# Kernel optimization log

Measured on AMD Instinct MI355X. Metric: run time of the kernel, lower is better.

The kernel has to match this reference:

```python
import jax, jax.numpy as jnp
import numpy as np

B, L, E, H, NL = 2, 1024, 1024, 16, 3
D = E // H
SCALE = D ** -0.5
EPS = 1e-5


def rmsnorm(x, g):
    return x * jax.lax.rsqrt(jnp.mean(x * x, axis=-1, keepdims=True) + EPS) * g


def rope(x, cos, sin):
    # x: (B, m*L, H, D); cos/sin: (L, D). Tile cos/sin to the growing KV length
    # (the source broadcasts rel_pos over the concatenated cache).
    m = x.shape[1] // cos.shape[0]
    c = jnp.tile(cos, (m, 1))[None, :, None, :]
    s = jnp.tile(sin, (m, 1))[None, :, None, :]
    x1, x2 = jnp.split(x, 2, axis=-1)
    rot = jnp.concatenate([-x2, x1], axis=-1)  # rotate_half convention
    return x * c + rot * s


def setup_inputs() -> dict:
    key = jax.random.key(0)
    ks = jax.random.split(key, 8)
    x = jax.random.normal(ks[0], (B, L, E), jnp.float32)
    inv_freq = 1.0 / (10000.0 ** (jnp.arange(0, D, 2, dtype=jnp.float32) / D))
    t = jnp.arange(L, dtype=jnp.float32)[:, None] * inv_freq[None, :]  # (L, D/2)
    cos = jnp.concatenate([jnp.cos(t), jnp.cos(t)], axis=-1)
    sin = jnp.concatenate([jnp.sin(t), jnp.sin(t)], axis=-1)
    attn_mask = jnp.where(jnp.tril(jnp.ones((L, L), bool)), 0.0, -jnp.inf).astype(jnp.float32)
    w_scale = E ** -0.5  # ~kaiming_uniform fan_in magnitude
    Wq = jax.random.normal(ks[1], (NL, E, E), jnp.float32) * w_scale
    Wk = jax.random.normal(ks[2], (NL, E, E), jnp.float32) * w_scale
    Wv = jax.random.normal(ks[3], (NL, E, E), jnp.float32) * w_scale
    Wo = jax.random.normal(ks[4], (E, E), jnp.float32) * w_scale
    lambdas = jax.random.normal(ks[5], (NL,), jnp.float32)
    g_ln = jnp.ones((NL, E), jnp.float32)
    g_final = jnp.ones((E,), jnp.float32)
    alpha = jnp.ones((1,), jnp.float32)
    return dict(x=x, cos=cos, sin=sin, attn_mask=attn_mask, Wq=Wq, Wk=Wk, Wv=Wv,
                g_ln=g_ln, lambdas=lambdas, Wo=Wo, g_final=g_final, alpha=alpha)


def reference(x, cos, sin, attn_mask, Wq, Wk, Wv, g_ln, lambdas, Wo, g_final, alpha):
    # lambda weights: sigmoid then non-affine LayerNorm across the NL layers
    s = jax.nn.sigmoid(lambdas)
    lw = (s - s.mean()) * jax.lax.rsqrt(s.var() + EPS)

    acc_k, acc_v = [], []
    outs = []
    for i in range(NL):
        q = (x @ Wq[i].T).reshape(B, L, H, D)
        k = (x @ Wk[i].T).reshape(B, L, H, D)
        v = (x @ Wv[i].T).reshape(B, L, H, D)
        if i > 0:  # prepend-current growing KV cache (source concatenates [k, accumulated])
            k = jnp.concatenate([k] + acc_k, axis=1)
            v = jnp.concatenate([v] + acc_v, axis=1)
        q = rope(q, cos, sin)
        k = rope(k, cos, sin)
        KV = k.shape[1]
        scores = jnp.einsum('bqhd,bkhd->bhqk', q * SCALE, k)  # (B,H,L,KV)
        if i == 0:
            m = attn_mask
        else:  # source fills everything past tgt_len with -inf
            m = jnp.concatenate(
                [attn_mask, jnp.full((L, KV - L), -jnp.inf, attn_mask.dtype)], axis=1)
        w = jax.nn.softmax(scores + m, axis=-1)
        a = jnp.einsum('bhqk,bkhd->bqhd', w, v).reshape(B, L, E)
        outs.append(rmsnorm(a, g_ln[i]) * lw[i])
        acc_k.append(k)  # stores the full concatenated, roped k (lengths 1L,2L,4L)
        acc_v.append(v)
    combined = outs[0] + outs[1] + outs[2]
    out = rmsnorm(combined + alpha * x, g_final)
    return out @ Wo.T
```

## Files before the change

### kernel.cpp

```cpp
#include <hip/hip_runtime.h>


#define B_  2
#define L_  1024
#define E_  1024
#define H_  16
#define NL_ 3
#define D_  64

typedef __bf16 bf16_t;
typedef __bf16 bf16x8 __attribute__((ext_vector_type(8)));
typedef __bf16 bf16x4 __attribute__((ext_vector_type(4)));
typedef float  f32x4  __attribute__((ext_vector_type(4)));

#define NEG_INF (-__builtin_inff())

typedef const __attribute__((address_space(1))) void* gas_ptr;
typedef __attribute__((address_space(3))) void* las_ptr;

#define GLD_LDS16(gp, lp) \
  __builtin_amdgcn_global_load_lds((gas_ptr)(gp), (las_ptr)(lp), 16, 0, 0)

__global__ __launch_bounds__(256) void cvt_k(
    const float* __restrict__ s0, const float* __restrict__ s1,
    const float* __restrict__ s2, const float* __restrict__ s3,
    const float* __restrict__ s4, bf16_t* __restrict__ d0,
    bf16_t* __restrict__ d1, bf16_t* __restrict__ d2, bf16_t* __restrict__ d3,
    bf16_t* __restrict__ d4)
{
  const int seg = blockIdx.y;
  const float* s;
  bf16_t* d;
  int n;
  if (seg == 0)      { s = s0; d = d0; n = 3145728; }
  else if (seg == 1) { s = s1; d = d1; n = 3145728; }
  else if (seg == 2) { s = s2; d = d2; n = 3145728; }
  else if (seg == 3) { s = s3; d = d3; n = 1048576; }
  else               { s = s4; d = d4; n = 2097152; }
  const int i = (blockIdx.x * 256 + threadIdx.x) * 4;
  if (i < n) {
    const float4 v = *(const float4*)(s + i);
    bf16x4 o;
    o[0] = (bf16_t)v.x; o[1] = (bf16_t)v.y; o[2] = (bf16_t)v.z; o[3] = (bf16_t)v.w;
    *(bf16x4*)(d + i) = o;
  }
}

template <int EPI>
__global__ __launch_bounds__(256) void gemm_k(
    const bf16_t* __restrict__ X, const bf16_t* __restrict__ W0,
    const bf16_t* __restrict__ W1, const bf16_t* __restrict__ W2,
    const float* __restrict__ cosb, const float* __restrict__ sinb,
    bf16_t* __restrict__ qk, bf16_t* __restrict__ vt, float* __restrict__ outf)
{
  __shared__ bf16_t smem[128 * 128];
  bf16_t* Xs = smem;
  bf16_t* Ws = smem + 8192;
  const int tid = threadIdx.x;
  const int lane = tid & 63;
  const int w = tid >> 6;
  const int q4 = lane >> 4, l15 = lane & 15;
  const int l7 = l15 & 7;
  const int row0 = blockIdx.x * 128;

  int g, tileN;
  const bf16_t* Wb;
  if (EPI == 0) {
    g = blockIdx.y >> 3;
    tileN = blockIdx.y & 7;
    const int t = g % 3, il = g / 3;
    Wb = (t == 0 ? W0 : (t == 1 ? W1 : W2)) + (size_t)il * E_ * E_;
  } else {
    g = 0;
    tileN = blockIdx.y;
    Wb = W0;
  }
  const int col0 = tileN * 128;
  const int rA = (w & 1) * 64;
  const int cB = (w >> 1) * 64;

  const int srow = tid >> 3;
  const int scol = (((tid & 7) ^ (srow & 7)) << 3);

  f32x4 acc[4][4] = {};

  for (int k0 = 0; k0 < E_; k0 += 64) {
    __syncthreads();
#pragma unroll
    for (int it = 0; it < 4; ++it) {
      const int flat = it * 2048 + tid * 8;
      const int r = it * 32 + srow;
      GLD_LDS16(X + (size_t)(row0 + r) * E_ + k0 + scol, &Xs[flat]);
      GLD_LDS16(Wb + (size_t)(col0 + r) * E_ + k0 + scol, &Ws[flat]);
    }
    __syncthreads();
#pragma unroll
    for (int kk = 0; kk < 2; ++kk) {
      bf16x8 a[4], b[4];
      const int cg = ((kk * 4 + q4) ^ l7) << 3;
#pragma unroll
      for (int mi = 0; mi < 4; ++mi)
        a[mi] = *(const bf16x8*)&Xs[(rA + mi * 16 + l15) * 64 + cg];
#pragma unroll
      for (int ni = 0; ni < 4; ++ni)
        b[ni] = *(const bf16x8*)&Ws[(cB + ni * 16 + l15) * 64 + cg];
#pragma unroll
      for (int mi = 0; mi < 4; ++mi)
#pragma unroll
        for (int ni = 0; ni < 4; ++ni)
          acc[mi][ni] =
              __builtin_amdgcn_mfma_f32_16x16x32_bf16(a[mi], b[ni], acc[mi][ni], 0, 0, 0);
    }
  }

  if (EPI == 0) {
    const int t = g % 3, il = g / 3;
    if (t < 2) {
      const int slot = il * 2 + t;
      const int h = tileN * 2 + (w >> 1);
      const float post = (t == 0) ? 0.18033688011112042f : 1.0f;
#pragma unroll
      for (int mi = 0; mi < 4; ++mi) {
#pragma unroll
        for (int reg = 0; reg < 4; ++reg) {
          const int m = row0 + rA + mi * 16 + q4 * 4 + reg;
          const int b = m >> 10, l = m & (L_ - 1);
#pragma unroll
          for (int ni = 0; ni < 4; ++ni) {
            const int d = ni * 16 + l15;
            const float v0 = acc[mi][ni][reg];
            const float part = acc[mi][ni ^ 2][reg];
            const float rot = (d < 32) ? -part : part;
            const float v = (v0 * cosb[l * D_ + d] + rot * sinb[l * D_ + d]) * post;
            qk[(((size_t)slot * B_ + b) * H_ + h) * ((size_t)L_ * D_) +
               (size_t)l * D_ + d] = (bf16_t)v;
          }
        }
      }
    } else {
      const int n_l = tid >> 1, lh = tid & 1;
      const int h = tileN * 2 + (n_l >> 6), d = n_l & 63;
      const int bb = row0 >> 10;
      __syncthreads();
#pragma unroll
      for (int p = 0; p < 2; ++p) {
        if ((w & 1) == p) {
#pragma unroll
          for (int mi = 0; mi < 4; ++mi)
#pragma unroll
            for (int reg = 0; reg < 4; ++reg)
#pragma unroll
              for (int ni = 0; ni < 4; ++ni)
                smem[(cB + ni * 16 + l15) * 72 + mi * 16 + q4 * 4 + reg] =
                    (bf16_t)acc[mi][ni][reg];
        }
        __syncthreads();
        const int l0 = (row0 & (L_ - 1)) + p * 64 + lh * 32;
        bf16_t* gp = vt + (((size_t)il * B_ + bb) * H_ + h) * ((size_t)D_ * L_) +
                     (size_t)d * L_ + l0;
        const bf16_t* sp = &smem[n_l * 72 + lh * 32];
#pragma unroll
        for (int c = 0; c < 4; ++c)
          *(bf16x8*)(gp + c * 8) = *(const bf16x8*)(sp + c * 8);
        if (p == 0) __syncthreads();
      }
    }
  } else {
#pragma unroll
    for (int mi = 0; mi < 4; ++mi) {
#pragma unroll
      for (int reg = 0; reg < 4; ++reg) {
        const int m = row0 + rA + mi * 16 + q4 * 4 + reg;
#pragma unroll
        for (int ni = 0; ni < 4; ++ni) {
          const int n = col0 + cB + ni * 16 + l15;
          outf[(size_t)m * E_ + n] = acc[mi][ni][reg];
        }
      }
    }
  }
}

__global__ __launch_bounds__(256) void attn_k(const bf16_t* __restrict__ qk,
                                              const bf16_t* __restrict__ vt,
                                              bf16_t* __restrict__ attn)
{
  __shared__ bf16_t Ks[2][64 * 64];
  __shared__ bf16_t Vts[2][64 * 64];
  __shared__ bf16_t Ps[4][16 * 72];

  const int tid = threadIdx.x, lane = tid & 63, w = tid >> 6;
  const int q4 = lane >> 4, l15 = lane & 15;
  const int x = blockIdx.x;
  const int by = blockIdx.y;
  const int h = by & 15, b = (by >> 4) & 1, i = by >> 5;
  const size_t HD = (size_t)L_ * D_;
  const bf16_t* Qp = qk + (((size_t)(i * 2 + 0) * B_ + b) * H_ + h) * HD;
  const bf16_t* Kp = qk + (((size_t)(i * 2 + 1) * B_ + b) * H_ + h) * HD;
  const bf16_t* Vp = vt + (((size_t)i * B_ + b) * H_ + h) * HD;

  const int srow = tid >> 3;
  const int sg = tid & 7;
  const int scol = (sg ^ (srow & 7)) * 8;

  bf16x8 ones;
#pragma unroll
  for (int jj = 0; jj < 8; ++jj) ones[jj] = (bf16_t)1.0f;

#pragma unroll 1
  for (int ph = 0; ph < 2; ++ph) {
    const int qt = ph == 0 ? (15 - x) : x;

    bf16x8 aq[2];
#pragma unroll
    for (int kk = 0; kk < 2; ++kk)
      aq[kk] = *(const bf16x8*)(Qp + (size_t)(qt * 64 + w * 16 + l15) * 64 +
                                kk * 32 + q4 * 8);

    if (ph == 1) __syncthreads();
#pragma unroll
    for (int it = 0; it < 2; ++it) {
      const int flat = it * 2048 + tid * 8;
      const int r = it * 32 + srow;
      GLD_LDS16(Kp + r * 64 + scol, &Ks[0][flat]);
      GLD_LDS16(Vp + (size_t)r * L_ + scol, &Vts[0][flat]);
    }

    f32x4 o[4] = {};
    f32x4 lacc = {};

#pragma unroll 1
    for (int j = 0; j <= qt; ++j) {
      __syncthreads();
      const int cur = j & 1;
      if (j < qt) {
        const int nxt = cur ^ 1;
#pragma unroll
        for (int it = 0; it < 2; ++it) {
          const int flat = it * 2048 + tid * 8;
          const int r = it * 32 + srow;
          GLD_LDS16(Kp + (j + 1) * 4096 + r * 64 + scol, &Ks[nxt][flat]);
          GLD_LDS16(Vp + (size_t)r * L_ + (j + 1) * 64 + scol, &Vts[nxt][flat]);
        }
      }

      f32x4 s[4] = {};
#pragma unroll
      for (int kk = 0; kk < 2; ++kk) {
#pragma unroll
        for (int ni = 0; ni < 4; ++ni) {
          const bf16x8 bk =
              *(const bf16x8*)&Ks[cur][(ni * 16 + l15) * 64 +
                                       (((kk * 4 + q4) ^ (l15 & 7)) << 3)];
          s[ni] = __builtin_amdgcn_mfma_f32_16x16x32_bf16(aq[kk], bk, s[ni], 0, 0, 0);
        }
      }

      if (j == qt) {
#pragma unroll
        for (int reg = 0; reg < 4; ++reg)
#pragma unroll
          for (int ni = 0; ni < 4; ++ni)
            if (ni * 16 + l15 > w * 16 + q4 * 4 + reg) s[ni][reg] = NEG_INF;
      }

#pragma unroll
      for (int reg = 0; reg < 4; ++reg)
#pragma unroll
        for (int ni = 0; ni < 4; ++ni)
          Ps[w][(q4 * 4 + reg) * 72 + ni * 16 + l15] = (bf16_t)exp2f(s[ni][reg]);
      asm volatile("s_waitcnt lgkmcnt(0)" ::: "memory");

#pragma unroll
      for (int kk = 0; kk < 2; ++kk) {
        const bf16x8 ap = *(const bf16x8*)&Ps[w][l15 * 72 + kk * 32 + q4 * 8];
        lacc = __builtin_amdgcn_mfma_f32_16x16x32_bf16(ap, ones, lacc, 0, 0, 0);
#pragma unroll
        for (int di = 0; di < 4; ++di) {
          const bf16x8 bv =
              *(const bf16x8*)&Vts[cur][(di * 16 + l15) * 64 +
                                        (((kk * 4 + q4) ^ (l15 & 7)) << 3)];
          o[di] = __builtin_amdgcn_mfma_f32_16x16x32_bf16(ap, bv, o[di], 0, 0, 0);
        }
      }
    }

    const int row_base = (i * B_ + b) * L_ + qt * 64 + w * 16 + q4 * 4;
#pragma unroll
    for (int reg = 0; reg < 4; ++reg) {
      const float inv = 1.f / lacc[reg];
      const int r = row_base + reg;
#pragma unroll
      for (int di = 0; di < 4; ++di)
        attn[(size_t)r * E_ + h * 64 + di * 16 + l15] = (bf16_t)(o[di][reg] * inv);
    }
  }
}

__device__ __forceinline__ float block_sum(float v, float* sm)
{
#pragma unroll
  for (int off = 32; off > 0; off >>= 1) v += __shfl_xor(v, off);
  const int w = threadIdx.x >> 6;
  __syncthreads();
  if ((threadIdx.x & 63) == 0) sm[w] = v;
  __syncthreads();
  return sm[0] + sm[1] + sm[2] + sm[3];
}

__global__ __launch_bounds__(256) void combine_k(
    const bf16_t* __restrict__ attn, const float* __restrict__ x,
    const float* __restrict__ g_ln, const float* __restrict__ lambdas,
    const float* __restrict__ g_final, const float* __restrict__ alphap,
    bf16_t* __restrict__ xn)
{
  __shared__ float sm[4];
  const int row = blockIdx.x;
  const int tid = threadIdx.x;

  float sg[3], lw[3];
#pragma unroll
  for (int i = 0; i < 3; ++i) sg[i] = 1.f / (1.f + expf(-lambdas[i]));
  const float mean = (sg[0] + sg[1] + sg[2]) * (1.f / 3.f);
  const float var = ((sg[0] - mean) * (sg[0] - mean) + (sg[1] - mean) * (sg[1] - mean) +
                     (sg[2] - mean) * (sg[2] - mean)) * (1.f / 3.f);
  const float rv = rsqrtf(var + 1e-5f);
#pragma unroll
  for (int i = 0; i < 3; ++i) lw[i] = (sg[i] - mean) * rv;

  const float av = alphap[0];
  float c[4];
#pragma unroll
  for (int k = 0; k < 4; ++k) {
    const int e = tid + k * 256;
    c[k] = av * x[(size_t)row * E_ + e];
  }

  for (int i = 0; i < 3; ++i) {
    float a[4];
    float ss = 0.f;
#pragma unroll
    for (int k = 0; k < 4; ++k) {
      const int e = tid + k * 256;
      a[k] = (float)attn[((size_t)i * (B_ * L_) + row) * E_ + e];
      ss += a[k] * a[k];
    }
    ss = block_sum(ss, sm);
    const float rinv = rsqrtf(ss * (1.f / (float)E_) + 1e-5f);
#pragma unroll
    for (int k = 0; k < 4; ++k) {
      const int e = tid + k * 256;
      c[k] += a[k] * rinv * g_ln[i * E_ + e] * lw[i];
    }
  }

  float ss = 0.f;
#pragma unroll
  for (int k = 0; k < 4; ++k) ss += c[k] * c[k];
  ss = block_sum(ss, sm);
  const float rinv = rsqrtf(ss * (1.f / (float)E_) + 1e-5f);
#pragma unroll
  for (int k = 0; k < 4; ++k) {
    const int e = tid + k * 256;
    xn[(size_t)row * E_ + e] = (bf16_t)(c[k] * rinv * g_final[e]);
  }
}

extern "C" void kernel_launch(void* const* d_in, const int* in_sizes, int n_in,
                              void* d_out, int out_size, void* d_ws, size_t ws_size,
                              hipStream_t stream)
{
  const float* x       = (const float*)d_in[0];
  const float* cosb    = (const float*)d_in[1];
  const float* sinb    = (const float*)d_in[2];
  const float* Wq      = (const float*)d_in[4];
  const float* Wk      = (const float*)d_in[5];
  const float* Wv      = (const float*)d_in[6];
  const float* g_ln    = (const float*)d_in[7];
  const float* lambdas = (const float*)d_in[8];
  const float* Wo      = (const float*)d_in[9];
  const float* g_final = (const float*)d_in[10];
  const float* alphap  = (const float*)d_in[11];

  bf16_t* qk    = (bf16_t*)d_ws;
  bf16_t* VT    = (bf16_t*)((char*)d_ws + 25165824);
  bf16_t* attnb = (bf16_t*)((char*)d_ws + 37748736);
  bf16_t* Wqb   = (bf16_t*)((char*)d_ws + 50331648);
  bf16_t* Wkb   = Wqb + 3145728;
  bf16_t* Wvb   = Wkb + 3145728;
  bf16_t* Wob   = (bf16_t*)((char*)d_ws + 69206016);
  bf16_t* xb    = (bf16_t*)((char*)d_ws + 71303168);
  bf16_t* xnb   = (bf16_t*)d_ws;
  float*  out   = (float*)d_out;

  cvt_k<<<dim3(3072, 5), 256, 0, stream>>>(Wq, Wk, Wv, Wo, x, Wqb, Wkb, Wvb, Wob, xb);
  gemm_k<0><<<dim3(16, 72), 256, 0, stream>>>(xb, Wqb, Wkb, Wvb, cosb, sinb,
                                              qk, VT, nullptr);
  attn_k<<<dim3(8, 96), 256, 0, stream>>>(qk, VT, attnb);
  combine_k<<<dim3(B_ * L_), 256, 0, stream>>>(attnb, x, g_ln, lambdas, g_final,
                                               alphap, xnb);
  gemm_k<1><<<dim3(16, 8), 256, 0, stream>>>(xnb, Wob, Wob, Wob, cosb, sinb,
                                             nullptr, nullptr, out);
}
```

Measured before the change: 240.5 us.

## Load K/V fragments directly from global memory instead of LDS double-buffering

Removes the shared-memory double-buffered K and V tiles, which were staged with global_load_lds, along with their block-wide barriers. Each wave now loads its MFMA operand fragments for K and V straight from global memory into registers. This drops LDS traffic and __syncthreads, but every wave re-reads the same K/V tile from global/L2 and the load latency is no longer overlapped by a prefetch, so the kernel depends more on cache bandwidth and latency.

```diff
diff --git a/kernel.cpp b/kernel.cpp
--- a/kernel.cpp
+++ b/kernel.cpp
@@ -185,8 +185,6 @@
                                               const bf16_t* __restrict__ vt,
                                               bf16_t* __restrict__ attn)
 {
-  __shared__ bf16_t Ks[2][64 * 64];
-  __shared__ bf16_t Vts[2][64 * 64];
   __shared__ bf16_t Ps[4][16 * 72];
 
   const int tid = threadIdx.x, lane = tid & 63, w = tid >> 6;
@@ -199,9 +197,8 @@
   const bf16_t* Kp = qk + (((size_t)(i * 2 + 1) * B_ + b) * H_ + h) * HD;
   const bf16_t* Vp = vt + (((size_t)i * B_ + b) * H_ + h) * HD;
 
-  const int srow = tid >> 3;
-  const int sg = tid & 7;
-  const int scol = (sg ^ (srow & 7)) * 8;
+  const int kfrag = (l15 * 64) + q4 * 8;
+  const size_t vfrag = (size_t)l15 * L_ + q4 * 8;
 
   bf16x8 ones;
 #pragma unroll
@@ -217,44 +214,35 @@
       aq[kk] = *(const bf16x8*)(Qp + (size_t)(qt * 64 + w * 16 + l15) * 64 +
                                 kk * 32 + q4 * 8);
 
-    if (ph == 1) __syncthreads();
-#pragma unroll
-    for (int it = 0; it < 2; ++it) {
-      const int flat = it * 2048 + tid * 8;
-      const int r = it * 32 + srow;
-      GLD_LDS16(Kp + r * 64 + scol, &Ks[0][flat]);
-      GLD_LDS16(Vp + (size_t)r * L_ + scol, &Vts[0][flat]);
-    }
-
     f32x4 o[4] = {};
     f32x4 lacc = {};
 
 #pragma unroll 1
     for (int j = 0; j <= qt; ++j) {
-      __syncthreads();
-      const int cur = j & 1;
-      if (j < qt) {
-        const int nxt = cur ^ 1;
-#pragma unroll
-        for (int it = 0; it < 2; ++it) {
-          const int flat = it * 2048 + tid * 8;
-          const int r = it * 32 + srow;
-          GLD_LDS16(Kp + (j + 1) * 4096 + r * 64 + scol, &Ks[nxt][flat]);
-          GLD_LDS16(Vp + (size_t)r * L_ + (j + 1) * 64 + scol, &Vts[nxt][flat]);
-        }
-      }
+      const bf16_t* kbase = Kp + j * 4096 + kfrag;
+      const bf16_t* vbase = Vp + j * 64 + vfrag;
+
+      bf16x8 bk[2][4];
+#pragma unroll
+      for (int kk = 0; kk < 2; ++kk)
+#pragma unroll
+        for (int ni = 0; ni < 4; ++ni)
+          bk[kk][ni] = *(const bf16x8*)(kbase + ni * 1024 + kk * 32);
 
       f32x4 s[4] = {};
 #pragma unroll
-      for (int kk = 0; kk < 2; ++kk) {
-#pragma unroll
-        for (int ni = 0; ni < 4; ++ni) {
-          const bf16x8 bk =
-              *(const bf16x8*)&Ks[cur][(ni * 16 + l15) * 64 +
-                                       (((kk * 4 + q4) ^ (l15 & 7)) << 3)];
-          s[ni] = __builtin_amdgcn_mfma_f32_16x16x32_bf16(aq[kk], bk, s[ni], 0, 0, 0);
-        }
-      }
+      for (int kk = 0; kk < 2; ++kk)
+#pragma unroll
+        for (int ni = 0; ni < 4; ++ni)
+          s[ni] = __builtin_amdgcn_mfma_f32_16x16x32_bf16(aq[kk], bk[kk][ni],
+                                                          s[ni], 0, 0, 0);
+
+      bf16x8 bv[2][4];
+#pragma unroll
+      for (int kk = 0; kk < 2; ++kk)
+#pragma unroll
+        for (int di = 0; di < 4; ++di)
+          bv[kk][di] = *(const bf16x8*)(vbase + (size_t)di * 16384 + kk * 32);
 
       if (j == qt) {
 #pragma unroll
@@ -276,12 +264,9 @@
         const bf16x8 ap = *(const bf16x8*)&Ps[w][l15 * 72 + kk * 32 + q4 * 8];
         lacc = __builtin_amdgcn_mfma_f32_16x16x32_bf16(ap, ones, lacc, 0, 0, 0);
 #pragma unroll
-        for (int di = 0; di < 4; ++di) {
-          const bf16x8 bv =
-              *(const bf16x8*)&Vts[cur][(di * 16 + l15) * 64 +
-                                        (((kk * 4 + q4) ^ (l15 & 7)) << 3)];
-          o[di] = __builtin_amdgcn_mfma_f32_16x16x32_bf16(ap, bv, o[di], 0, 0, 0);
-        }
+        for (int di = 0; di < 4; ++di)
+          o[di] = __builtin_amdgcn_mfma_f32_16x16x32_bf16(ap, bv[kk][di],
+                                                          o[di], 0, 0, 0);
       }
     }
 
```

Result: slower. 294.8 us (+22.6%).
